# Kernel tuning notes

Hardware: AMD Instinct MI355X
Metric: run time of the kernel (lower is better)

## Reference

```python
import jax, jax.numpy as jnp
import numpy as np
from jax import lax

NAMES = ['k', 'v', 'q', 'eta', 'alpha', 'memory']
RES = {'k': True, 'v': True, 'q': True, 'eta': False, 'alpha': False, 'memory': True}
CHUNK = 16


def _mlp(x, st, residual):
    # x: (B,C,d_in); st W1:(B,d_out,d_hid) W2:(B,d_hid,d_in) b1:(B,d_out) b2:(B,d_hid)
    h = jax.nn.silu(jnp.einsum('bcd,bhd->bch', x, st['W2']) + st['b2'][:, None, :])
    out = jnp.einsum('bch,boh->bco', h, st['W1']) + st['b1'][:, None, :]
    return x + out if residual else out


def _dgd_grads(x, target, st, residual):
    # manual chain rule for L = (1/2C)||M(x)-target||^2
    C = x.shape[1]
    pre = jnp.einsum('bcd,bhd->bch', x, st['W2']) + st['b2'][:, None, :]
    sig = jax.nn.sigmoid(pre)
    h = pre * sig  # silu
    pred = jnp.einsum('bch,boh->bco', h, st['W1']) + st['b1'][:, None, :]
    if residual:
        pred = x + pred
    error = (pred - target) / C  # (B,C,d_out)
    dW1 = jnp.einsum('bco,bch->boh', error, h)
    db1 = error.sum(axis=1)
    dl_dh = jnp.einsum('bco,boh->bch', error, st['W1'])
    silu_grad = sig * (1.0 + pre * (1.0 - sig))
    dl_dpre = dl_dh * silu_grad
    dW2 = jnp.einsum('bch,bcd->bhd', dl_dpre, x)
    db2 = dl_dpre.sum(axis=1)
    return {'W1': dW1, 'W2': dW2, 'b1': db1, 'b2': db2}


def _clamp(w):
    B = w.shape[0]
    flat = w.reshape(B, -1)
    norm = jnp.linalg.norm(flat, axis=1)
    max_n = np.sqrt(flat.shape[1]).astype(np.float32)
    scale = jnp.minimum(max_n / (norm + 1e-8), 1.0)
    return w * scale.reshape((B,) + (1,) * (w.ndim - 1))


def _l2norm(x):
    return x / jnp.maximum(jnp.linalg.norm(x, axis=-1, keepdims=True), 1e-12)


def _titans(x, mods, in_W, in_b, out_W, out_b, ln_g, ln_b):
    B, T, _ = x.shape
    C = CHUNK
    NC = T // C
    z = x @ in_W.T + in_b  # (B,T,d_memory)
    zc = z.reshape(B, NC, C, -1).transpose(1, 0, 2, 3)  # (NC,B,C,d)

    states = {}
    for name in NAMES:
        W1, b1, W2, b2 = mods[name]
        states[name] = {
            'W1': jnp.broadcast_to(W1, (B,) + W1.shape),
            'b1': jnp.broadcast_to(b1, (B,) + b1.shape),
            'W2': jnp.broadcast_to(W2, (B,) + W2.shape),
            'b2': jnp.broadcast_to(b2, (B,) + b2.shape),
        }

    def step(st, z_chunk):
        k = _mlp(z_chunk, st['k'], True)
        v = _mlp(z_chunk, st['v'], True)
        q = _mlp(z_chunk, st['q'], True)
        eta = jax.nn.sigmoid(_mlp(z_chunk, st['eta'], False))    # (B,C,1)
        alpha = jax.nn.sigmoid(_mlp(z_chunk, st['alpha'], False))
        k = _l2norm(k)
        q = _l2norm(q)
        o = _mlp(q, st['memory'], True)
        ea = eta.mean(axis=1)    # (B,1)
        aa = alpha.mean(axis=1)  # (B,1)
        new = {}
        for name in NAMES:
            s = st[name]
            res = RES[name]
            v_hat = lax.stop_gradient(_mlp(v, s, res))
            g = _dgd_grads(k, v_hat, s, res)
            ns = {}
            for pn in ('W1', 'W2', 'b1', 'b2'):
                gr = g[pn]
                a = aa.reshape((aa.shape[0],) + (1,) * (gr.ndim - 1))
                e = ea.reshape((ea.shape[0],) + (1,) * (gr.ndim - 1))
                ns[pn] = _clamp(a * s[pn] - e * gr)
            new[name] = ns
        new = jax.tree.map(lax.stop_gradient, new)  # bptt_depth=0 detach
        return new, o

    _, outs = lax.scan(step, states, zc)  # outs: (NC,B,C,d)
    out = outs.transpose(1, 0, 2, 3).reshape(B, T, -1)
    mu = out.mean(axis=-1, keepdims=True)
    var = out.var(axis=-1, keepdims=True)
    out = (out - mu) / jnp.sqrt(var + 1e-5) * ln_g + ln_b
    return out @ out_W.T + out_b


def setup_inputs() -> dict:
    key = jax.random.key(0)
    B, T, Dm = 4, 2048, 1024
    Dmem = 1024
    ks = jax.random.split(key, 10)
    inp = {'x': jax.random.normal(ks[0], (B, T, Dm), jnp.float32)}
    d_outs = {'k': Dmem, 'v': Dmem, 'q': Dmem, 'eta': 1, 'alpha': 1, 'memory': Dmem}
    b1_special = {'eta': -3.0, 'alpha': 3.0}
    for i, (m, do) in enumerate(d_outs.items()):
        inp[f'{m}_W1'] = jnp.zeros((do, Dmem), jnp.float32)
        inp[f'{m}_b1'] = jnp.full((do,), b1_special.get(m, 0.0), jnp.float32)
        inp[f'{m}_W2'] = (jax.random.normal(ks[1 + i], (Dmem, Dm), jnp.float32)
                          * np.sqrt(2.0 / Dm).astype(np.float32))
        inp[f'{m}_b2'] = jnp.zeros((Dmem,), jnp.float32)
    inp['in_W'] = jax.random.normal(ks[7], (Dmem, Dm), jnp.float32) * 0.02
    inp['in_b'] = jnp.zeros((Dmem,), jnp.float32)
    inp['out_W'] = jax.random.normal(ks[8], (Dm, Dmem), jnp.float32) * 0.02
    inp['out_b'] = jnp.zeros((Dm,), jnp.float32)
    inp['ln_g'] = jnp.ones((Dmem,), jnp.float32)
    inp['ln_b'] = jnp.zeros((Dmem,), jnp.float32)
    return inp


def reference(x, k_W1, k_b1, k_W2, k_b2, v_W1, v_b1, v_W2, v_b2,
              q_W1, q_b1, q_W2, q_b2, eta_W1, eta_b1, eta_W2, eta_b2,
              alpha_W1, alpha_b1, alpha_W2, alpha_b2,
              memory_W1, memory_b1, memory_W2, memory_b2,
              in_W, in_b, out_W, out_b, ln_g, ln_b):
    mods = {
        'k': (k_W1, k_b1, k_W2, k_b2),
        'v': (v_W1, v_b1, v_W2, v_b2),
        'q': (q_W1, q_b1, q_W2, q_b2),
        'eta': (eta_W1, eta_b1, eta_W2, eta_b2),
        'alpha': (alpha_W1, alpha_b1, alpha_W2, alpha_b2),
        'memory': (memory_W1, memory_b1, memory_W2, memory_b2),
    }
    return _titans(x, mods, in_W, in_b, out_W, out_b, ln_g, ln_b)
```

## Files before the change

kernel.cpp:

```cpp
#include <hip/hip_runtime.h>
#include <math.h>

#define DI __device__ __forceinline__

namespace {

typedef unsigned short u16;
typedef unsigned int u32;
typedef __attribute__((ext_vector_type(8))) short bf8;
typedef __attribute__((ext_vector_type(4))) float f4;

DI f4 MFB(bf8 a, bf8 b, f4 c) { return __builtin_amdgcn_mfma_f32_16x16x32_bf16(a, b, c, 0, 0, 0); }

constexpr int DOUTS[6] = {1024, 1024, 1024, 1, 1, 1024};
constexpr int BIGM[4] = {0, 1, 2, 5};

constexpr long SZ_BIGM = 2100224, SZ_SMALLM = 1051648;
constexpr long MODOFF[6] = {0, SZ_BIGM, 2 * SZ_BIGM, 3 * SZ_BIGM,
                            3 * SZ_BIGM + SZ_SMALLM, 3 * SZ_BIGM + 2 * SZ_SMALLM};
constexpr long BSTRIDE = 3 * SZ_BIGM + 2 * SZ_SMALLM + SZ_BIGM;

constexpr long OFF_Z     = 0;
constexpr long OFF_STATE = 8388608;
constexpr long OFF_SPRE5 = OFF_STATE + 4 * BSTRIDE;
constexpr long OFF_KVQ   = OFF_SPRE5 + 327680;
constexpr long OFF_SPREV = OFF_KVQ + 196608;
constexpr long OFF_PREK  = OFF_SPREV + 393216;
constexpr long OFF_SPREK = OFF_PREK + 393216;
constexpr long OFF_SPREO = OFF_SPREK + 393216;
constexpr long OFF_ERR   = OFF_SPREO + 65536;
constexpr long OFF_DLP   = OFF_ERR + 393216;
constexpr long OFF_RSSQ  = OFF_DLP + 393216;
constexpr long OFF_EA    = OFF_RSSQ + 128;
constexpr long OFF_SCALE = OFF_EA + 8;
constexpr long OFF_SUMSQ = OFF_SCALE + 96;
constexpr long OFF_FLAG  = OFF_SUMSQ + 96;
constexpr long WS_FLOATS = OFF_FLAG + 8;

struct InPtrs { const float* p[31]; };

DI float* modBase(float* ws, int b, int m) {
  return ws + OFF_STATE + (long)b * BSTRIDE + MODOFF[m];
}
DI float* vecp(float* base, int m) { return base + ((m == 3 || m == 4) ? 1048576 : 2097152); }
DI int sidx(int b, int m, int p) { return ((b * 6 + m) << 2) + p; }
DI float maxnf(int m, int p) {
  switch (p) {
    case 0: return sqrtf((float)(1024 * DOUTS[m]));
    case 1: return sqrtf((float)DOUTS[m]);
    case 2: return 1024.0f;
    default: return 32.0f;
  }
}
DI float sigm(float x) { return 1.0f / (1.0f + expf(-x)); }
DI float silu(float x) { return x * sigm(x); }
DI u16 f2bf(float x) {
  u32 u = __float_as_uint(x);
  return (u16)((u + 0x7fffu + ((u >> 16) & 1u)) >> 16);
}

DI void sumsqReduce(float ss, float* slack, float* dst) {
#pragma unroll
  for (int st = 32; st >= 1; st >>= 1) ss += __shfl_xor(ss, st);
  const int tid = threadIdx.x;
  if ((tid & 63) == 0) slack[tid >> 6] = ss;
  __syncthreads();
  if (tid == 0) atomicAdd(dst, slack[0] + slack[1] + slack[2] + slack[3]);
  __syncthreads();
}

DI void split3v(const float v[8], bf8& p0, bf8& p1, bf8& p2) {
#pragma unroll
  for (int i = 0; i < 8; i++) {
    const u32 u = __float_as_uint(v[i]);
    const float f0 = __uint_as_float(u & 0xffff0000u);
    const float r1 = v[i] - f0;
    const u32 u1 = __float_as_uint(r1);
    const float f1 = __uint_as_float(u1 & 0xffff0000u);
    const float r2 = r1 - f1;
    p0[i] = (short)(u >> 16);
    p1[i] = (short)(u1 >> 16);
    p2[i] = (short)f2bf(r2);
  }
}
DI void split3p(const float* p, bf8& p0, bf8& p1, bf8& p2) {
  const float4 a = *(const float4*)p, b = *(const float4*)(p + 4);
  const float v[8] = {a.x, a.y, a.z, a.w, b.x, b.y, b.z, b.w};
  split3v(v, p0, p1, p2);
}

__global__ void k_probe(float* ws) {
  const int l = threadIdx.x, cl = l & 15, kq = l >> 4;
  bf8 af, bf_;
#pragma unroll
  for (int i = 0; i < 8; i++) { af[i] = 0; bf_[i] = 0; }
  if (kq == 0) {
    af[0] = (short)f2bf((float)(cl + 1));
    bf_[0] = (short)f2bf((float)(128 * (cl + 1)));
  }
  f4 d = MFB(af, bf_, f4{0.f, 0.f, 0.f, 0.f});
  bool m0 = true, m1 = true;
#pragma unroll
  for (int r = 0; r < 4; r++) {
    m0 = m0 && (d[r] == (float)((kq * 4 + r + 1) * 128 * (cl + 1)));
    m1 = m1 && (d[r] == (float)((cl + 1) * 128 * (kq * 4 + r + 1)));
  }
  const unsigned long long b0 = __ballot(m0), b1 = __ballot(m1);
  if (l == 0) ws[OFF_FLAG] = (b0 == ~0ull) ? 0.f : ((b1 == ~0ull) ? 1.f : 0.f);
}

template <class EF>
DI void mcK1(float* sm, const float* __restrict__ X, const float* __restrict__ W,
             int n0, int flg, EF&& ef) {
  const int tid = threadIdx.x, g = tid >> 6, l = tid & 63, cl = l & 15, kq = l >> 4;
  f4 acc = {0.f, 0.f, 0.f, 0.f};
  const float* Xr = X + (long)cl * 1024 + g * 256 + kq * 8;
  const float* Wr = W + (long)(n0 + cl) * 1024 + g * 256 + kq * 8;
#pragma unroll 2
  for (int ch = 0; ch < 8; ch++) {
    bf8 x0, x1, x2, w0, w1, w2;
    split3p(Xr + ch * 32, x0, x1, x2);
    split3p(Wr + ch * 32, w0, w1, w2);
    acc = MFB(x2, w0, acc); acc = MFB(x1, w1, acc); acc = MFB(x0, w2, acc);
    acc = MFB(x1, w0, acc); acc = MFB(x0, w1, acc); acc = MFB(x0, w0, acc);
  }
  *(f4*)(sm + g * 256 + l * 4) = acc;
  __syncthreads();
  const int le = tid >> 2, re = tid & 3;
  const float v = sm[le * 4 + re] + sm[256 + le * 4 + re] +
                  sm[512 + le * 4 + re] + sm[768 + le * 4 + re];
  const int ccl = le & 15, ckq = le >> 4;
  const int c = flg ? ccl : ckq * 4 + re;
  const int n = n0 + (flg ? ckq * 4 + re : ccl);
  ef(c, n, v);
}

template <class EF>
DI void mcK2(float* sm, const float* __restrict__ X1, const float* __restrict__ X2,
             const float* __restrict__ W, int n0, int flg, EF&& ef) {
  const int tid = threadIdx.x, g = tid >> 6, l = tid & 63, cl = l & 15, kq = l >> 4;
  f4 a1 = {0.f, 0.f, 0.f, 0.f}, a2 = {0.f, 0.f, 0.f, 0.f};
  const float* X1r = X1 + (long)cl * 1024 + g * 256 + kq * 8;
  const float* X2r = X2 + (long)cl * 1024 + g * 256 + kq * 8;
  const float* Wr = W + (long)(n0 + cl) * 1024 + g * 256 + kq * 8;
#pragma unroll 2
  for (int ch = 0; ch < 8; ch++) {
    bf8 w0, w1, w2, x0, x1, x2, y0, y1, y2;
    split3p(Wr + ch * 32, w0, w1, w2);
    split3p(X1r + ch * 32, x0, x1, x2);
    split3p(X2r + ch * 32, y0, y1, y2);
    a1 = MFB(x2, w0, a1); a1 = MFB(x1, w1, a1); a1 = MFB(x0, w2, a1);
    a1 = MFB(x1, w0, a1); a1 = MFB(x0, w1, a1); a1 = MFB(x0, w0, a1);
    a2 = MFB(y2, w0, a2); a2 = MFB(y1, w1, a2); a2 = MFB(y0, w2, a2);
    a2 = MFB(y1, w0, a2); a2 = MFB(y0, w1, a2); a2 = MFB(y0, w0, a2);
  }
  *(f4*)(sm + g * 256 + l * 4) = a1;
  *(f4*)(sm + 1024 + g * 256 + l * 4) = a2;
  __syncthreads();
  const int le = tid >> 2, re = tid & 3;
  const float v1 = sm[le * 4 + re] + sm[256 + le * 4 + re] +
                   sm[512 + le * 4 + re] + sm[768 + le * 4 + re];
  const float v2 = sm[1024 + le * 4 + re] + sm[1280 + le * 4 + re] +
                   sm[1536 + le * 4 + re] + sm[1792 + le * 4 + re];
  const int ccl = le & 15, ckq = le >> 4;
  const int c = flg ? ccl : ckq * 4 + re;
  const int n = n0 + (flg ? ckq * 4 + re : ccl);
  ef(c, n, v1, v2);
}

template <class EF>
DI void mcK1t(float* sm, const float* __restrict__ E, const float* __restrict__ W1,
              int h0, int flg, EF&& ef) {
  const int tid = threadIdx.x, g = tid >> 6, l = tid & 63, cl = l & 15, kq = l >> 4;
  f4 acc = {0.f, 0.f, 0.f, 0.f};
  const float* Er = E + (long)cl * 1024 + g * 256 + kq * 8;
  const float* Wc = W1 + (long)(g * 256 + kq * 8) * 1024 + h0 + cl;
#pragma unroll 2
  for (int ch = 0; ch < 8; ch++) {
    bf8 x0, x1, x2, w0, w1, w2;
    split3p(Er + ch * 32, x0, x1, x2);
    float v[8];
#pragma unroll
    for (int i = 0; i < 8; i++) v[i] = Wc[(long)(ch * 32 + i) * 1024];
    split3v(v, w0, w1, w2);
    acc = MFB(x2, w0, acc); acc = MFB(x1, w1, acc); acc = MFB(x0, w2, acc);
    acc = MFB(x1, w0, acc); acc = MFB(x0, w1, acc); acc = MFB(x0, w0, acc);
  }
  *(f4*)(sm + g * 256 + l * 4) = acc;
  __syncthreads();
  const int le = tid >> 2, re = tid & 3;
  const float v = sm[le * 4 + re] + sm[256 + le * 4 + re] +
                  sm[512 + le * 4 + re] + sm[768 + le * 4 + re];
  const int ccl = le & 15, ckq = le >> 4;
  const int c = flg ? ccl : ckq * 4 + re;
  const int h = h0 + (flg ? ckq * 4 + re : ccl);
  ef(c, h, v);
}


__global__ __launch_bounds__(256) void k_p0(float* ws, InPtrs in) {
  const long i = threadIdx.x + (long)blockIdx.x * 256;
  if (i < 96) { ws[OFF_SCALE + i] = 1.f; return; }
  if (i < 192) { ws[OFF_SUMSQ + (i - 96)] = 0.f; return; }
  if (i < 320) { ws[OFF_RSSQ + (i - 192)] = 0.f; return; }
  const long j = i - 320;
  if (j < 24 * 2048) {
    const int bm = (int)(j >> 11), q = (int)(j & 2047);
    const int b = bm / 6, m = bm % 6;
    float* vc = vecp(modBase(ws, b, m), m);
    if (q < 1024) { if (q < DOUTS[m]) vc[q] = in.p[2 + 4 * m][q]; }
    else vc[1024 + (q - 1024)] = in.p[4 + 4 * m][q - 1024];
    return;
  }
  const long j2 = j - 49152;
  if (j2 < 8192) {
    const int e = (int)(j2 >> 10), b = e >> 1, m = 3 + (e & 1);
    const int h = (int)(j2 & 1023);
    vecp(modBase(ws, b, m), m)[2048 + h] = in.p[1 + 4 * m][h];
  }
}

__global__ __launch_bounds__(256) void k_pc(float* ws, InPtrs in) {
  const int bid = blockIdx.x, job = bid >> 9, sub = bid & 511;
  const long e0 = (long)sub * 2048 + threadIdx.x * 8;
  int m; bool w1;
  if (job < 6) { m = job; w1 = false; }
  else { m = BIGM[job - 6]; w1 = true; }
  const float* src = in.p[(w1 ? 1 : 3) + 4 * m];
  const float4 a = *(const float4*)(src + e0);
  const float4 b4 = *(const float4*)(src + e0 + 4);
#pragma unroll
  for (int q = 0; q < 4; q++) {
    float* dst = modBase(ws, q, m) + (w1 ? 1048576 : 0);
    *(float4*)(dst + e0) = a;
    *(float4*)(dst + e0 + 4) = b4;
  }
}

__global__ __launch_bounds__(256) void k_gbig(const float* __restrict__ X,
                                              const float* __restrict__ A,
                                              const float* __restrict__ bias,
                                              float* __restrict__ Y,
                                              const float* flagp) {
  __shared__ float sm[1024];
  const int bid = blockIdx.x, nb = bid & 63;
  const long rb = bid >> 6;
  const int flg = (int)flagp[0];
  const float* Xr = X + rb * 16 * 1024;
  float* Yr = Y + rb * 16 * 1024;
  mcK1(sm, Xr, A, nb * 16, flg, [&](int c, int n, float v) {
    Yr[(long)c * 1024 + n] = v + bias[n];
  });
}


__global__ __launch_bounds__(256) void k_s0(float* ws) {
  const int i = threadIdx.x;
  if (i < 96) {
    const float ssv = ws[OFF_SUMSQ + i];
    const int p = i & 3, m = (i >> 2) % 6;
    ws[OFF_SCALE + i] = fminf(maxnf(m, p) / (sqrtf(ssv) + 1e-8f), 1.0f);
    ws[OFF_SUMSQ + i] = 0.f;
  } else if (i < 224) {
    ws[OFF_RSSQ + (i - 96)] = 0.f;
  }
}

__global__ __launch_bounds__(256) void k_s1(float* ws, int t) {
  __shared__ float sm[1024];
  const int bid = blockIdx.x, n0 = (bid & 63) * 16, m = (bid >> 6) % 5, b = bid / 320;
  const int flg = (int)ws[OFF_FLAG];
  const float* zc = ws + OFF_Z + ((long)b * 2048 + (long)t * 16) * 1024;
  float* base = modBase(ws, b, m);
  const float cW2 = ws[OFF_SCALE + sidx(b, m, 2)], cb2 = ws[OFF_SCALE + sidx(b, m, 3)];
  const float* b2v = vecp(base, m) + 1024;
  float* Y = ws + OFF_SPRE5 + ((long)b * 5 + m) * 16384;
  mcK1(sm, zc, base, n0, flg, [&](int c, int n, float v) {
    Y[(long)c * 1024 + n] = silu(fmaf(cW2, v, cb2 * b2v[n]));
  });
}

__global__ __launch_bounds__(256) void k_s2(float* ws, int t) {
  __shared__ float sm[1024 + 16 + 64];
  float* smr = sm + 1024;
  float* sm2 = sm + 1040;
  const int tid = threadIdx.x, bid = blockIdx.x;
  if (bid < 768) {
    const int n0 = (bid & 63) * 16, m = (bid >> 6) % 3, b = bid / 192;
    const int flg = (int)ws[OFF_FLAG];
    if (tid < 16) smr[tid] = 0.f;
    const float* spre = ws + OFF_SPRE5 + ((long)b * 5 + m) * 16384;
    float* base = modBase(ws, b, m);
    const float* zc = ws + OFF_Z + ((long)b * 2048 + (long)t * 16) * 1024;
    const float cW1 = ws[OFF_SCALE + sidx(b, m, 0)], cb1 = ws[OFF_SCALE + sidx(b, m, 1)];
    const float* b1v = vecp(base, m);
    float* out = ws + OFF_KVQ + ((long)b * 3 + m) * 16384;
    const bool sq = (m != 1);
    mcK1(sm, spre, base + 1048576, n0, flg, [&](int c, int n, float v) {
      const float val = fmaf(cW1, v, fmaf(cb1, b1v[n], zc[(long)c * 1024 + n]));
      out[(long)c * 1024 + n] = val;
      if (sq) atomicAdd(&smr[c], val * val);
    });
    __syncthreads();
    if (sq && tid < 16)
      atomicAdd(ws + OFF_RSSQ + (long)b * 32 + (m == 0 ? 0 : 16) + tid, smr[tid]);
  } else {
    const int e = bid - 768, b = e >> 1, m = 3 + (e & 1);
    const float* spre = ws + OFF_SPRE5 + ((long)b * 5 + m) * 16384;
    float* base = modBase(ws, b, m);
    const float* w1 = vecp(base, m) + 2048;
    float av[16];
#pragma unroll
    for (int c = 0; c < 16; c++) av[c] = 0.f;
    for (int jj = 0; jj < 4; jj++) {
      const int h = tid + 256 * jj;
      const float w = w1[h];
#pragma unroll
      for (int c = 0; c < 16; c++) av[c] = fmaf(spre[c * 1024 + h], w, av[c]);
    }
#pragma unroll
    for (int st = 1; st < 64; st <<= 1)
#pragma unroll
      for (int c = 0; c < 16; c++) av[c] += __shfl_xor(av[c], st);
    if ((tid & 63) == 0) {
      const int w4 = tid >> 6;
#pragma unroll
      for (int c = 0; c < 16; c++) sm2[w4 * 16 + c] = av[c];
    }
    __syncthreads();
    if (tid == 0) {
      const float cW1 = ws[OFF_SCALE + sidx(b, m, 0)], cb1 = ws[OFF_SCALE + sidx(b, m, 1)];
      const float b10 = vecp(base, m)[0];
      float s = 0.f;
      for (int c = 0; c < 16; c++) {
        const float tot = sm2[c] + sm2[16 + c] + sm2[32 + c] + sm2[48 + c];
        s += sigm(fmaf(cW1, tot, cb1 * b10));
      }
      ws[OFF_EA + ((m == 3) ? 0 : 4) + b] = s * 0.0625f;
    }
  }
}

__global__ __launch_bounds__(256) void k_s3(float* ws) {
  __shared__ float sm[2048 + 16];
  float* sminv = sm + 2048;
  const int bid = blockIdx.x, tid = threadIdx.x;
  const int flg = (int)ws[OFF_FLAG];
  if (bid < 1536) {
    const int n0 = (bid & 63) * 16, m = (bid >> 6) % 6, b = bid / 384;
    if (tid < 16)
      sminv[tid] = 1.f / fmaxf(sqrtf(ws[OFF_RSSQ + (long)b * 32 + tid]), 1e-12f);
    const float* vX = ws + OFF_KVQ + ((long)b * 3 + 1) * 16384;
    const float* kX = ws + OFF_KVQ + ((long)b * 3 + 0) * 16384;
    float* base = modBase(ws, b, m);
    const float cW2 = ws[OFF_SCALE + sidx(b, m, 2)], cb2 = ws[OFF_SCALE + sidx(b, m, 3)];
    const float* b2v = vecp(base, m) + 1024;
    float* Ysv = ws + OFF_SPREV + ((long)b * 6 + m) * 16384;
    float* Yk = ws + OFF_PREK + ((long)b * 6 + m) * 16384;
    float* Ysk = ws + OFF_SPREK + ((long)b * 6 + m) * 16384;
    mcK2(sm, vX, kX, base, n0, flg, [&](int c, int n, float v1, float v2) {
      const float bb = cb2 * b2v[n];
      Ysv[(long)c * 1024 + n] = silu(fmaf(cW2, v1, bb));
      const float pk = fmaf(cW2 * sminv[c], v2, bb);
      Yk[(long)c * 1024 + n] = pk;
      Ysk[(long)c * 1024 + n] = silu(pk);
    });
  } else {
    const int id = bid - 1536, n0 = (id & 63) * 16, b = id >> 6;
    if (tid < 16)
      sminv[tid] = 1.f / fmaxf(sqrtf(ws[OFF_RSSQ + (long)b * 32 + 16 + tid]), 1e-12f);
    const float* qX = ws + OFF_KVQ + ((long)b * 3 + 2) * 16384;
    float* base = modBase(ws, b, 5);
    const float cW2 = ws[OFF_SCALE + sidx(b, 5, 2)], cb2 = ws[OFF_SCALE + sidx(b, 5, 3)];
    const float* b2v = vecp(base, 5) + 1024;
    float* Y = ws + OFF_SPREO + (long)b * 16384;
    mcK1(sm, qX, base, n0, flg, [&](int c, int n, float v) {
      Y[(long)c * 1024 + n] = silu(fmaf(cW2 * sminv[c], v, cb2 * b2v[n]));
    });
  }
}

__global__ __launch_bounds__(256) void k_s4(float* ws, int t) {
  __shared__ float sm[2048 + 16 + 128];
  float* sminv = sm + 2048;
  float* sm4 = sm + 2064;
  const int tid = threadIdx.x, bid = blockIdx.x;
  if (bid < 1024) {
    const int n0 = (bid & 63) * 16, mi = (bid >> 6) & 3, b = bid >> 8;
    const int m = BIGM[mi];
    const int flg = (int)ws[OFF_FLAG];
    if (tid < 16)
      sminv[tid] = 1.f / fmaxf(sqrtf(ws[OFF_RSSQ + (long)b * 32 + tid]), 1e-12f);
    const float* sprev = ws + OFF_SPREV + ((long)b * 6 + m) * 16384;
    const float* sprek = ws + OFF_SPREK + ((long)b * 6 + m) * 16384;
    float* base = modBase(ws, b, m);
    const float cW1 = ws[OFF_SCALE + sidx(b, m, 0)], cb1 = ws[OFF_SCALE + sidx(b, m, 1)];
    const float* b1v = vecp(base, m);
    const float* vraw = ws + OFF_KVQ + ((long)b * 3 + 1) * 16384;
    const float* kraw = ws + OFF_KVQ + ((long)b * 3 + 0) * 16384;
    float* errP = ws + OFF_ERR + ((long)b * 6 + m) * 16384;
    mcK2(sm, sprev, sprek, base + 1048576, n0, flg, [&](int c, int n, float v1, float v2) {
      const float bbb = cb1 * b1v[n];
      const float vh = fmaf(cW1, v1, bbb + vraw[(long)c * 1024 + n]);
      const float pr = fmaf(cW1, v2, bbb + kraw[(long)c * 1024 + n] * sminv[c]);
      errP[(long)c * 1024 + n] = (pr - vh) * 0.0625f;
    });
  } else if (bid < 1280) {
    const int id = bid - 1024, n0 = (id & 63) * 16, b = id >> 6;
    const int flg = (int)ws[OFF_FLAG];
    if (tid < 16)
      sminv[tid] = 1.f / fmaxf(sqrtf(ws[OFF_RSSQ + (long)b * 32 + 16 + tid]), 1e-12f);
    const float* spreo = ws + OFF_SPREO + (long)b * 16384;
    float* base = modBase(ws, b, 5);
    const float cW1 = ws[OFF_SCALE + sidx(b, 5, 0)], cb1 = ws[OFF_SCALE + sidx(b, 5, 1)];
    const float* b1v = vecp(base, 5);
    const float* qraw = ws + OFF_KVQ + ((long)b * 3 + 2) * 16384;
    float* zc = ws + OFF_Z + ((long)b * 2048 + (long)t * 16) * 1024;
    mcK1(sm, spreo, base + 1048576, n0, flg, [&](int c, int n, float v) {
      zc[(long)c * 1024 + n] = fmaf(cW1, v, cb1 * b1v[n] + qraw[(long)c * 1024 + n] * sminv[c]);
    });
  } else {
    const int id = bid - 1280, b = id >> 1, m = 3 + (id & 1);
    const float* sprev = ws + OFF_SPREV + ((long)b * 6 + m) * 16384;
    const float* sprek = ws + OFF_SPREK + ((long)b * 6 + m) * 16384;
    float* base = modBase(ws, b, m);
    const float* w1 = vecp(base, m) + 2048;
    float av[16], ap[16];
#pragma unroll
    for (int c = 0; c < 16; c++) { av[c] = 0.f; ap[c] = 0.f; }
    for (int jj = 0; jj < 4; jj++) {
      const int h = tid + 256 * jj;
      const float w = w1[h];
#pragma unroll
      for (int c = 0; c < 16; c++) {
        av[c] = fmaf(sprev[c * 1024 + h], w, av[c]);
        ap[c] = fmaf(sprek[c * 1024 + h], w, ap[c]);
      }
    }
#pragma unroll
    for (int st = 1; st < 64; st <<= 1)
#pragma unroll
      for (int c = 0; c < 16; c++) {
        av[c] += __shfl_xor(av[c], st);
        ap[c] += __shfl_xor(ap[c], st);
      }
    if ((tid & 63) == 0) {
      const int w4 = tid >> 6;
#pragma unroll
      for (int c = 0; c < 16; c++) { sm4[w4 * 32 + c] = av[c]; sm4[w4 * 32 + 16 + c] = ap[c]; }
    }
    __syncthreads();
    if (tid == 0) {
      const float cW1 = ws[OFF_SCALE + sidx(b, m, 0)], cb1 = ws[OFF_SCALE + sidx(b, m, 1)];
      const float b10 = vecp(base, m)[0];
      float* errP = ws + OFF_ERR + ((long)b * 6 + m) * 16384;
      for (int c = 0; c < 16; c++) {
        const float sv = sm4[c] + sm4[32 + c] + sm4[64 + c] + sm4[96 + c];
        const float sp = sm4[16 + c] + sm4[48 + c] + sm4[80 + c] + sm4[112 + c];
        errP[c * 1024] = (fmaf(cW1, sp, cb1 * b10) - fmaf(cW1, sv, cb1 * b10)) * 0.0625f;
      }
    }
  }
}

__global__ __launch_bounds__(256) void k_s5(float* ws) {
  __shared__ float sm[1024];
  const int tid = threadIdx.x, bid = blockIdx.x;
  if (bid < 1024) {
    const int h0 = (bid & 63) * 16, mi = (bid >> 6) & 3, b = bid >> 8;
    const int m = BIGM[mi];
    const int flg = (int)ws[OFF_FLAG];
    float* base = modBase(ws, b, m);
    const float* errP = ws + OFF_ERR + ((long)b * 6 + m) * 16384;
    const float cW1 = ws[OFF_SCALE + sidx(b, m, 0)];
    const float* prek = ws + OFF_PREK + ((long)b * 6 + m) * 16384;
    float* dlp = ws + OFF_DLP + ((long)b * 6 + m) * 16384;
    mcK1t(sm, errP, base + 1048576, h0, flg, [&](int c, int h, float v) {
      const float pre = prek[(long)c * 1024 + h];
      const float sg = sigm(pre);
      dlp[(long)c * 1024 + h] = cW1 * v * (sg * (1.f + pre * (1.f - sg)));
    });
  } else {
    const int e = bid - 1024, sub = e & 3, bm = e >> 2, b = bm >> 1, m = 3 + (bm & 1);
    const float cW1 = ws[OFF_SCALE + sidx(b, m, 0)];
    const float* errP = ws + OFF_ERR + ((long)b * 6 + m) * 16384;
    const float* prek = ws + OFF_PREK + ((long)b * 6 + m) * 16384;
    const float* w1 = vecp(modBase(ws, b, m), m) + 2048;
    float* dlp = ws + OFF_DLP + ((long)b * 6 + m) * 16384;
    for (int i = tid; i < 4096; i += 256) {
      const long idx = (long)sub * 4096 + i;
      const int c = (int)(idx >> 10), h = (int)(idx & 1023);
      const float pre = prek[idx];
      const float sg = sigm(pre);
      dlp[idx] = errP[c * 1024] * cW1 * w1[h] * (sg * (1.f + pre * (1.f - sg)));
    }
  }
}

__global__ __launch_bounds__(256) void k_s6(float* ws) {
  __shared__ float sm[64 * 20 + 8];
  float* slack = sm + 64 * 20;
  const int tid = threadIdx.x, bid = blockIdx.x;
  if (bid < 640) {
    const bool isW2 = bid < 384;
    int b, m, r0, scaleIdx;
    float* W;
    float4 fac[16];
    const float* tsrc;
    if (isW2) {
      const int bm = bid >> 4;
      b = bm / 6; m = bm % 6; r0 = (bid & 15) * 64;
      W = modBase(ws, b, m);
      scaleIdx = sidx(b, m, 2);
      tsrc = ws + OFF_DLP + ((long)b * 6 + m) * 16384;
      const float* kraw = ws + OFF_KVQ + ((long)b * 3) * 16384;
#pragma unroll
      for (int c = 0; c < 16; c++) {
        const float inv = 1.f / fmaxf(sqrtf(ws[OFF_RSSQ + (long)b * 32 + c]), 1e-12f);
        const float4 kk = *(const float4*)(kraw + (long)c * 1024 + tid * 4);
        fac[c].x = kk.x * inv; fac[c].y = kk.y * inv;
        fac[c].z = kk.z * inv; fac[c].w = kk.w * inv;
      }
    } else {
      const int id = bid - 384, bm = id >> 4;
      b = bm >> 2; m = BIGM[bm & 3]; r0 = (id & 15) * 64;
      W = modBase(ws, b, m) + 1048576;
      scaleIdx = sidx(b, m, 0);
      tsrc = ws + OFF_ERR + ((long)b * 6 + m) * 16384;
      const float* sprek = ws + OFF_SPREK + ((long)b * 6 + m) * 16384;
#pragma unroll
      for (int c = 0; c < 16; c++)
        fac[c] = *(const float4*)(sprek + (long)c * 1024 + tid * 4);
    }
    for (int f = tid; f < 1024; f += 256) {
      const int c = f >> 6, hh = f & 63;
      sm[hh * 20 + c] = tsrc[(long)c * 1024 + r0 + hh];
    }
    __syncthreads();
    const float ea = ws[OFF_EA + b], aa = ws[OFF_EA + 4 + b];
    const float ac = aa * ws[OFF_SCALE + scaleIdx];
    float ss = 0.f;
#pragma unroll 1
    for (int hh = 0; hh < 64; hh++) {
      const float4 q0 = *(const float4*)(sm + hh * 20);
      const float4 q1 = *(const float4*)(sm + hh * 20 + 4);
      const float4 q2 = *(const float4*)(sm + hh * 20 + 8);
      const float4 q3 = *(const float4*)(sm + hh * 20 + 12);
      float4 g = {0.f, 0.f, 0.f, 0.f};
#pragma unroll
      for (int c = 0; c < 16; c++) {
        const float4 qq = c < 4 ? q0 : (c < 8 ? q1 : (c < 12 ? q2 : q3));
        const float dv = (&qq.x)[c & 3];
        g.x = fmaf(dv, fac[c].x, g.x);
        g.y = fmaf(dv, fac[c].y, g.y);
        g.z = fmaf(dv, fac[c].z, g.z);
        g.w = fmaf(dv, fac[c].w, g.w);
      }
      float4* Wp = (float4*)(W + (size_t)(r0 + hh) * 1024 + tid * 4);
      float4 w = *Wp;
      w.x = fmaf(ac, w.x, -ea * g.x);
      w.y = fmaf(ac, w.y, -ea * g.y);
      w.z = fmaf(ac, w.z, -ea * g.z);
      w.w = fmaf(ac, w.w, -ea * g.w);
      *Wp = w;
      ss = fmaf(w.x, w.x, fmaf(w.y, w.y, fmaf(w.z, w.z, fmaf(w.w, w.w, ss))));
    }
    sumsqReduce(ss, slack, ws + OFF_SUMSQ + scaleIdx);
  } else if (bid < 688) {
    const int id = bid - 640;
    const int b = id / 12, r = id % 12, m = r >> 1, which = r & 1;
    const float ea = ws[OFF_EA + b], aa = ws[OFF_EA + 4 + b];
    float* vc = vecp(modBase(ws, b, m), m);
    float ss = 0.f;
    if (which == 0) {
      const int n = DOUTS[m];
      const float* errP = ws + OFF_ERR + ((long)b * 6 + m) * 16384;
      const float ac = aa * ws[OFF_SCALE + sidx(b, m, 1)];
      for (int o = tid; o < n; o += 256) {
        float gs = 0.f;
#pragma unroll
        for (int c = 0; c < 16; c++) gs += errP[c * 1024 + o];
        const float nw = fmaf(ac, vc[o], -ea * gs);
        vc[o] = nw;
        ss = fmaf(nw, nw, ss);
      }
      sumsqReduce(ss, slack, ws + OFF_SUMSQ + sidx(b, m, 1));
    } else {
      const float* dlpP = ws + OFF_DLP + ((long)b * 6 + m) * 16384;
      const float ac = aa * ws[OFF_SCALE + sidx(b, m, 3)];
      for (int h = tid; h < 1024; h += 256) {
        float gs = 0.f;
#pragma unroll
        for (int c = 0; c < 16; c++) gs += dlpP[c * 1024 + h];
        const float nw = fmaf(ac, vc[1024 + h], -ea * gs);
        vc[1024 + h] = nw;
        ss = fmaf(nw, nw, ss);
      }
      sumsqReduce(ss, slack, ws + OFF_SUMSQ + sidx(b, m, 3));
    }
  } else {
    const int e2 = bid - 688, b = e2 >> 1, m = 3 + (e2 & 1);
    const float ea = ws[OFF_EA + b], aa = ws[OFF_EA + 4 + b];
    float* vc = vecp(modBase(ws, b, m), m);
    const float* errP = ws + OFF_ERR + ((long)b * 6 + m) * 16384;
    const float* sprek = ws + OFF_SPREK + ((long)b * 6 + m) * 16384;
    const float ac = aa * ws[OFF_SCALE + sidx(b, m, 0)];
    float ss = 0.f;
    for (int h = tid; h < 1024; h += 256) {
      float gs = 0.f;
#pragma unroll
      for (int c = 0; c < 16; c++)
        gs = fmaf(errP[c * 1024], sprek[c * 1024 + h], gs);
      const float nw = fmaf(ac, vc[2048 + h], -ea * gs);
      vc[2048 + h] = nw;
      ss = fmaf(nw, nw, ss);
    }
    sumsqReduce(ss, slack, ws + OFF_SUMSQ + sidx(b, m, 0));
  }
}


__global__ __launch_bounds__(256) void k_ln(float* ws, const float* __restrict__ g,
                                            const float* __restrict__ bb) {
  __shared__ float sm[8];
  float* p = ws + OFF_Z + (long)blockIdx.x * 1024;
  const int tid = threadIdx.x;
  float s = 0.f, s2 = 0.f;
  for (int j = tid; j < 1024; j += 256) {
    const float v = p[j];
    s += v;
    s2 = fmaf(v, v, s2);
  }
#pragma unroll
  for (int st = 32; st >= 1; st >>= 1) { s += __shfl_xor(s, st); s2 += __shfl_xor(s2, st); }
  if ((tid & 63) == 0) { sm[tid >> 6] = s; sm[4 + (tid >> 6)] = s2; }
  __syncthreads();
  const float S = sm[0] + sm[1] + sm[2] + sm[3];
  const float S2 = sm[4] + sm[5] + sm[6] + sm[7];
  const float mu = S * (1.f / 1024.f);
  const float var = S2 * (1.f / 1024.f) - mu * mu;
  const float inv = 1.f / sqrtf(var + 1e-5f);
  for (int j = tid; j < 1024; j += 256) {
    p[j] = fmaf((p[j] - mu) * inv, g[j], bb[j]);
  }
}

}

extern "C" void kernel_launch(void* const* d_in, const int* in_sizes, int n_in,
                              void* d_out, int out_size, void* d_ws, size_t ws_size,
                              hipStream_t stream) {
  (void)in_sizes; (void)n_in; (void)out_size;
  if (ws_size < (size_t)WS_FLOATS * sizeof(float)) return;
  float* ws = (float*)d_ws;
  InPtrs ip;
  for (int i = 0; i < 31; i++) ip.p[i] = (const float*)d_in[i];

  k_probe<<<1, 64, 0, stream>>>(ws);
  k_p0<<<256, 256, 0, stream>>>(ws, ip);
  k_pc<<<5120, 256, 0, stream>>>(ws, ip);
  k_gbig<<<32768, 256, 0, stream>>>((const float*)d_in[0], (const float*)d_in[25],
                                    (const float*)d_in[26], ws + OFF_Z, ws + OFF_FLAG);

  for (int t = 0; t < 128; t++) {
    if (t) k_s0<<<1, 256, 0, stream>>>(ws);
    k_s1<<<1280, 256, 0, stream>>>(ws, t);
    k_s2<<<776, 256, 0, stream>>>(ws, t);
    k_s3<<<1792, 256, 0, stream>>>(ws);
    k_s4<<<1288, 256, 0, stream>>>(ws, t);
    k_s5<<<1056, 256, 0, stream>>>(ws);
    k_s6<<<696, 256, 0, stream>>>(ws);
  }

  k_ln<<<8192, 256, 0, stream>>>(ws, (const float*)d_in[29], (const float*)d_in[30]);
  k_gbig<<<32768, 256, 0, stream>>>(ws + OFF_Z, (const float*)d_in[27],
                                    (const float*)d_in[28], (float*)d_out, ws + OFF_FLAG);
}
```

Baseline: 25.37 ms.

## Defer weight updates into next step's matmul kernels with analytic norm tracking

```diff
diff --git a/kernel.cpp b/kernel.cpp
--- a/kernel.cpp
+++ b/kernel.cpp
@@ -20,22 +20,25 @@
                             3 * SZ_BIGM + SZ_SMALLM, 3 * SZ_BIGM + 2 * SZ_SMALLM};
 constexpr long BSTRIDE = 3 * SZ_BIGM + 2 * SZ_SMALLM + SZ_BIGM;
 
-constexpr long OFF_Z     = 0;
-constexpr long OFF_STATE = 8388608;
-constexpr long OFF_SPRE5 = OFF_STATE + 4 * BSTRIDE;
-constexpr long OFF_KVQ   = OFF_SPRE5 + 327680;
-constexpr long OFF_SPREV = OFF_KVQ + 196608;
-constexpr long OFF_PREK  = OFF_SPREV + 393216;
-constexpr long OFF_SPREK = OFF_PREK + 393216;
-constexpr long OFF_SPREO = OFF_SPREK + 393216;
-constexpr long OFF_ERR   = OFF_SPREO + 65536;
-constexpr long OFF_DLP   = OFF_ERR + 393216;
-constexpr long OFF_RSSQ  = OFF_DLP + 393216;
-constexpr long OFF_EA    = OFF_RSSQ + 128;
-constexpr long OFF_SCALE = OFF_EA + 8;
-constexpr long OFF_SUMSQ = OFF_SCALE + 96;
-constexpr long OFF_FLAG  = OFF_SUMSQ + 96;
-constexpr long WS_FLOATS = OFF_FLAG + 8;
+constexpr long OFF_Z       = 0;
+constexpr long OFF_STATE   = 8388608;
+constexpr long OFF_SPRE5   = OFF_STATE + 4 * BSTRIDE;
+constexpr long OFF_KVQ     = OFF_SPRE5 + 327680;
+constexpr long OFF_SPREV   = OFF_KVQ + 196608;
+constexpr long OFF_PREK    = OFF_SPREV + 393216;
+constexpr long OFF_SPREK   = OFF_PREK + 393216;
+constexpr long OFF_SPREO   = OFF_SPREK + 393216;
+constexpr long OFF_ERR     = OFF_SPREO + 65536;
+constexpr long OFF_DLP     = OFF_ERR + 393216;
+constexpr long OFF_PREKRAW = OFF_DLP + 393216;
+constexpr long OFF_RAWPK   = OFF_PREKRAW + 393216;
+constexpr long OFF_RSSQ    = OFF_RAWPK + 262144;
+constexpr long OFF_EA      = OFF_RSSQ + 256;
+constexpr long OFF_SCALE   = OFF_EA + 16;
+constexpr long OFF_SUMSQ   = OFF_SCALE + 192;
+constexpr long OFF_NORMSQ  = OFF_SUMSQ + 96;
+constexpr long OFF_FLAG    = OFF_NORMSQ + 96;
+constexpr long WS_FLOATS   = OFF_FLAG + 8;
 
 struct InPtrs { const float* p[31]; };
 
@@ -110,7 +113,7 @@
 }
 
 template <class EF>
-DI void mcK1(float* sm, const float* __restrict__ X, const float* __restrict__ W,
+DI void mcK1(float* sm, const float* __restrict__ X, const float* W,
              int n0, int flg, EF&& ef) {
   const int tid = threadIdx.x, g = tid >> 6, l = tid & 63, cl = l & 15, kq = l >> 4;
   f4 acc = {0.f, 0.f, 0.f, 0.f};
@@ -137,7 +140,7 @@
 
 template <class EF>
 DI void mcK2(float* sm, const float* __restrict__ X1, const float* __restrict__ X2,
-             const float* __restrict__ W, int n0, int flg, EF&& ef) {
+             const float* W, int n0, int flg, EF&& ef) {
   const int tid = threadIdx.x, g = tid >> 6, l = tid & 63, cl = l & 15, kq = l >> 4;
   f4 a1 = {0.f, 0.f, 0.f, 0.f}, a2 = {0.f, 0.f, 0.f, 0.f};
   const float* X1r = X1 + (long)cl * 1024 + g * 256 + kq * 8;
@@ -169,7 +172,7 @@
 }
 
 template <class EF>
-DI void mcK1t(float* sm, const float* __restrict__ E, const float* __restrict__ W1,
+DI void mcK1t(float* sm, const float* __restrict__ E, const float* W1,
               int h0, int flg, EF&& ef) {
   const int tid = threadIdx.x, g = tid >> 6, l = tid & 63, cl = l & 15, kq = l >> 4;
   f4 acc = {0.f, 0.f, 0.f, 0.f};
@@ -197,13 +200,39 @@
   ef(c, h, v);
 }
 
+DI void updTile(float* W, int n0, const float* coefS, const float4* fac,
+                float ac, float ea) {
+  const int tid = threadIdx.x;
+#pragma unroll 1
+  for (int hh = 0; hh < 16; hh++) {
+    float4 g = {0.f, 0.f, 0.f, 0.f};
+#pragma unroll
+    for (int c = 0; c < 16; c++) {
+      const float dv = coefS[c * 16 + hh];
+      g.x = fmaf(dv, fac[c].x, g.x);
+      g.y = fmaf(dv, fac[c].y, g.y);
+      g.z = fmaf(dv, fac[c].z, g.z);
+      g.w = fmaf(dv, fac[c].w, g.w);
+    }
+    float4* Wp = (float4*)(W + (size_t)(n0 + hh) * 1024 + tid * 4);
+    float4 w = *Wp;
+    w.x = fmaf(ac, w.x, -ea * g.x);
+    w.y = fmaf(ac, w.y, -ea * g.y);
+    w.z = fmaf(ac, w.z, -ea * g.z);
+    w.w = fmaf(ac, w.w, -ea * g.w);
+    *Wp = w;
+  }
+}
+
 
 __global__ __launch_bounds__(256) void k_p0(float* ws, InPtrs in) {
   const long i = threadIdx.x + (long)blockIdx.x * 256;
-  if (i < 96) { ws[OFF_SCALE + i] = 1.f; return; }
-  if (i < 192) { ws[OFF_SUMSQ + (i - 96)] = 0.f; return; }
-  if (i < 320) { ws[OFF_RSSQ + (i - 192)] = 0.f; return; }
-  const long j = i - 320;
+  if (i < 192) { ws[OFF_SCALE + i] = 1.f; return; }
+  if (i < 288) { ws[OFF_SUMSQ + (i - 192)] = 0.f; return; }
+  if (i < 384) { ws[OFF_NORMSQ + (i - 288)] = 0.f; return; }
+  if (i < 640) { ws[OFF_RSSQ + (i - 384)] = 0.f; return; }
+  if (i < 656) { ws[OFF_EA + (i - 640)] = 0.f; return; }
+  const long j = i - 656;
   if (j < 24 * 2048) {
     const int bm = (int)(j >> 11), q = (int)(j & 2047);
     const int b = bm / 6, m = bm % 6;
@@ -237,8 +266,30 @@
   }
 }
 
+__global__ __launch_bounds__(256) void k_pn(float* ws, InPtrs in) {
+  __shared__ float slack[8];
+  const int bid = blockIdx.x, job = bid >> 6, r0 = (bid & 63) * 16, tid = threadIdx.x;
+  const int m = (job < 5) ? job : job - 5;
+  const bool w1 = job >= 5;
+  const float* src = in.p[(w1 ? 1 : 3) + 4 * m];
+  float ss = 0.f;
+#pragma unroll 1
+  for (int r = 0; r < 16; r++) {
+    const float4 v = *(const float4*)(src + (size_t)(r0 + r) * 1024 + tid * 4);
+    ss = fmaf(v.x, v.x, fmaf(v.y, v.y, fmaf(v.z, v.z, fmaf(v.w, v.w, ss))));
+  }
+  sumsqReduce(ss, slack, ws + OFF_NORMSQ + sidx(0, m, w1 ? 0 : 2));
+}
+__global__ void k_pn2(float* ws) {
+  const int tid = threadIdx.x;
+  if (tid >= 24) return;
+  const int s = tid / 3, b = tid % 3 + 1;
+  const int m = (s < 5) ? s : s - 5, p = (s < 5) ? 2 : 0;
+  ws[OFF_NORMSQ + sidx(b, m, p)] = ws[OFF_NORMSQ + sidx(0, m, p)];
+}
+
 __global__ __launch_bounds__(256) void k_gbig(const float* __restrict__ X,
-                                              const float* __restrict__ A,
+                                              const float* A,
                                               const float* __restrict__ bias,
                                               float* __restrict__ Y,
                                               const float* flagp) {
@@ -254,56 +305,224 @@
 }
 
 
-__global__ __launch_bounds__(256) void k_s0(float* ws) {
-  const int i = threadIdx.x;
-  if (i < 96) {
-    const float ssv = ws[OFF_SUMSQ + i];
-    const int p = i & 3, m = (i >> 2) % 6;
-    ws[OFF_SCALE + i] = fminf(maxnf(m, p) / (sqrtf(ssv) + 1e-8f), 1.0f);
-    ws[OFF_SUMSQ + i] = 0.f;
-  } else if (i < 224) {
-    ws[OFF_RSSQ + (i - 96)] = 0.f;
+__global__ __launch_bounds__(256) void k_K0(float* ws, int t) {
+  __shared__ float sm[160];
+  const int tid = threadIdx.x, bid = blockIdx.x;
+  const int pc = t & 1, pp = (t - 1) & 1;
+  const float* eaP = ws + OFF_EA + pp * 8;
+  const float* sclP = ws + OFF_SCALE + pp * 96;
+  float* sclC = ws + OFF_SCALE + pc * 96;
+  if (bid < 32) {
+    int b, m, slot;
+    const float *A, *R;
+    const float *B;
+    bool isW2;
+    if (bid < 20) {
+      b = bid / 5; m = bid % 5; slot = sidx(b, m, 2); isW2 = true;
+      A = ws + OFF_DLP + ((long)b * 6 + m) * 16384;
+      R = ws + OFF_PREKRAW + ((long)b * 6 + m) * 16384;
+      B = ws + OFF_KVQ + (long)b * 3 * 16384;
+    } else {
+      const int id = bid - 20;
+      b = id / 3; m = id % 3; slot = sidx(b, m, 0); isW2 = false;
+      A = ws + OFF_ERR + ((long)b * 6 + m) * 16384;
+      R = ws + OFF_RAWPK + ((long)b * 4 + m) * 16384;
+      B = ws + OFF_SPREK + ((long)b * 6 + m) * 16384;
+    }
+    float dp = 0.f;
+    for (int i = tid; i < 16384; i += 256) dp = fmaf(A[i], R[i], dp);
+#pragma unroll
+    for (int st = 32; st >= 1; st >>= 1) dp += __shfl_xor(dp, st);
+    if ((tid & 63) == 0) sm[tid >> 6] = dp;
+    __syncthreads();
+    if (tid < 136) {
+      int c = 0, p = tid;
+      while (p >= 16 - c) { p -= 16 - c; c++; }
+      const int c2 = c + p;
+      float invc = 1.f, invc2 = 1.f;
+      if (isW2) {
+        const float* rs = ws + OFF_RSSQ + pp * 128 + (long)b * 32;
+        invc = 1.f / fmaxf(sqrtf(rs[c]), 1e-12f);
+        invc2 = 1.f / fmaxf(sqrtf(rs[c2]), 1e-12f);
+      }
+      float ga = 0.f, gb = 0.f;
+      const float *Ac = A + (long)c * 1024, *Ac2 = A + (long)c2 * 1024;
+      const float *Bc = B + (long)c * 1024, *Bc2 = B + (long)c2 * 1024;
+      for (int d = 0; d < 1024; d++) {
+        ga = fmaf(Ac[d], Ac2[d], ga);
+        gb = fmaf(Bc[d], Bc2[d], gb);
+      }
+      gb *= invc * invc2;
+      sm[8 + tid] = (c == c2 ? 1.f : 2.f) * ga * gb;
+    }
+    __syncthreads();
+    if (tid == 0) {
+      double dot = (double)sm[0] + sm[1] + sm[2] + sm[3];
+      double gg = 0.0;
+      for (int i = 0; i < 136; i++) gg += (double)sm[8 + i];
+      const double ea = (double)eaP[b], aa = (double)eaP[4 + b];
+      const double ac = aa * (double)sclP[slot];
+      double S = ac * ac * (double)ws[OFF_NORMSQ + slot] - 2.0 * ac * ea * dot +
+                 ea * ea * gg;
+      if (S < 0.0) S = 0.0;
+      ws[OFF_NORMSQ + slot] = (float)S;
+      sclC[slot] = fminf(maxnf(m, isW2 ? 2 : 0) / ((float)sqrt(S) + 1e-8f), 1.0f);
+    }
+  } else if (bid < 40) {
+    if (tid == 0) {
+      const int e = bid - 32, b = e >> 1, p = (e & 1) ? 0 : 2;
+      const int slot = sidx(b, 5, p);
+      const float S = ws[OFF_SUMSQ + slot];
+      sclC[slot] = fminf(maxnf(5, p) / (sqrtf(S) + 1e-8f), 1.0f);
+      ws[OFF_SUMSQ + slot] = 0.f;
+    }
+  } else if (bid < 96) {
+    const int id = bid - 40;
+    int b, m, kind;
+    if (id < 24) { b = id / 6; m = id % 6; kind = 0; }
+    else if (id < 48) { const int q = id - 24; b = q / 6; m = q % 6; kind = 1; }
+    else { const int q = id - 48; b = q >> 1; m = 3 + (q & 1); kind = 2; }
+    const float ea = eaP[b], aa = eaP[4 + b];
+    float* vc = vecp(modBase(ws, b, m), m);
+    if (kind == 0 && DOUTS[m] == 1) {
+      if (tid == 0) {
+        const float* errP = ws + OFF_ERR + ((long)b * 6 + m) * 16384;
+        float g = 0.f;
+        for (int c = 0; c < 16; c++) g += errP[c * 1024];
+        const float nv = fmaf(aa, vc[0], -ea * g);
+        const float sc = fminf(1.0f / (fabsf(nv) + 1e-8f), 1.0f);
+        vc[0] = sc * nv;
+      }
+      return;
+    }
+    float nv[4];
+    float ss = 0.f;
+    const int o = tid * 4;
+    if (kind == 0) {
+      const float* errP = ws + OFF_ERR + ((long)b * 6 + m) * 16384;
+#pragma unroll
+      for (int j = 0; j < 4; j++) {
+        float g = 0.f;
+        for (int c = 0; c < 16; c++) g += errP[c * 1024 + o + j];
+        nv[j] = fmaf(aa, vc[o + j], -ea * g);
+        ss = fmaf(nv[j], nv[j], ss);
+      }
+    } else if (kind == 1) {
+      const float* dlpP = ws + OFF_DLP + ((long)b * 6 + m) * 16384;
+#pragma unroll
+      for (int j = 0; j < 4; j++) {
+        float g = 0.f;
+        for (int c = 0; c < 16; c++) g += dlpP[c * 1024 + o + j];
+        nv[j] = fmaf(aa, vc[1024 + o + j], -ea * g);
+        ss = fmaf(nv[j], nv[j], ss);
+      }
+    } else {
+      const float* errP = ws + OFF_ERR + ((long)b * 6 + m) * 16384;
+      const float* sprek = ws + OFF_SPREK + ((long)b * 6 + m) * 16384;
+      float e0[16];
+#pragma unroll
+      for (int c = 0; c < 16; c++) e0[c] = errP[c * 1024];
+#pragma unroll
+      for (int j = 0; j < 4; j++) {
+        float g = 0.f;
+        for (int c = 0; c < 16; c++) g = fmaf(e0[c], sprek[c * 1024 + o + j], g);
+        nv[j] = fmaf(aa, vc[2048 + o + j], -ea * g);
+        ss = fmaf(nv[j], nv[j], ss);
+      }
+    }
+#pragma unroll
+    for (int st = 32; st >= 1; st >>= 1) ss += __shfl_xor(ss, st);
+    if ((tid & 63) == 0) sm[tid >> 6] = ss;
+    __syncthreads();
+    const float S = sm[0] + sm[1] + sm[2] + sm[3];
+    const float mx = (kind == 0) ? maxnf(m, 1) : 32.0f;
+    const float sc = fminf(mx / (sqrtf(S) + 1e-8f), 1.0f);
+    const long off = (kind == 0) ? 0 : (kind == 1 ? 1024 : 2048);
+#pragma unroll
+    for (int j = 0; j < 4; j++) vc[off + o + j] = sc * nv[j];
+  } else {
+    if (tid < 128) ws[OFF_RSSQ + pc * 128 + tid] = 0.f;
   }
 }
 
 __global__ __launch_bounds__(256) void k_s1(float* ws, int t) {
-  __shared__ float sm[1024];
-  const int bid = blockIdx.x, n0 = (bid & 63) * 16, m = (bid >> 6) % 5, b = bid / 320;
+  __shared__ float sm[1024 + 256];
+  const int bid = blockIdx.x, tid = threadIdx.x;
+  const int n0 = (bid & 63) * 16, m = (bid >> 6) % 5, b = bid / 320;
   const int flg = (int)ws[OFF_FLAG];
+  const int pc = t & 1, pp = (t - 1) & 1;
+  float* base = modBase(ws, b, m);
+  if (t > 0) {
+    const float* eaP = ws + OFF_EA + pp * 8;
+    const float ac = eaP[4 + b] * ws[OFF_SCALE + pp * 96 + sidx(b, m, 2)];
+    const float ea = eaP[b];
+    const float* kraw = ws + OFF_KVQ + (long)b * 3 * 16384;
+    const float* rs = ws + OFF_RSSQ + pp * 128 + (long)b * 32;
+    float4 fac[16];
+#pragma unroll
+    for (int c = 0; c < 16; c++) {
+      const float inv = 1.f / fmaxf(sqrtf(rs[c]), 1e-12f);
+      const float4 kk = *(const float4*)(kraw + (long)c * 1024 + tid * 4);
+      fac[c].x = kk.x * inv; fac[c].y = kk.y * inv;
+      fac[c].z = kk.z * inv; fac[c].w = kk.w * inv;
+    }
+    const float* dlpP = ws + OFF_DLP + ((long)b * 6 + m) * 16384;
+    sm[1024 + tid] = dlpP[(long)(tid >> 4) * 1024 + n0 + (tid & 15)];
+    __syncthreads();
+    updTile(base, n0, sm + 1024, fac, ac, ea);
+    __syncthreads();
+  }
   const float* zc = ws + OFF_Z + ((long)b * 2048 + (long)t * 16) * 1024;
-  float* base = modBase(ws, b, m);
-  const float cW2 = ws[OFF_SCALE + sidx(b, m, 2)], cb2 = ws[OFF_SCALE + sidx(b, m, 3)];
+  const float cW2 = ws[OFF_SCALE + pc * 96 + sidx(b, m, 2)];
   const float* b2v = vecp(base, m) + 1024;
   float* Y = ws + OFF_SPRE5 + ((long)b * 5 + m) * 16384;
   mcK1(sm, zc, base, n0, flg, [&](int c, int n, float v) {
-    Y[(long)c * 1024 + n] = silu(fmaf(cW2, v, cb2 * b2v[n]));
+    Y[(long)c * 1024 + n] = silu(fmaf(cW2, v, b2v[n]));
   });
 }
 
 __global__ __launch_bounds__(256) void k_s2(float* ws, int t) {
-  __shared__ float sm[1024 + 16 + 64];
-  float* smr = sm + 1024;
-  float* sm2 = sm + 1040;
+  __shared__ float sm[1024 + 256 + 16 + 64];
+  float* coefS = sm + 1024;
+  float* smr = sm + 1280;
+  float* sm2 = sm + 1296;
   const int tid = threadIdx.x, bid = blockIdx.x;
+  const int pc = t & 1, pp = (t - 1) & 1;
   if (bid < 768) {
     const int n0 = (bid & 63) * 16, m = (bid >> 6) % 3, b = bid / 192;
     const int flg = (int)ws[OFF_FLAG];
+    float* base = modBase(ws, b, m);
+    if (t > 0) {
+      const float* eaP = ws + OFF_EA + pp * 8;
+      const float ac = eaP[4 + b] * ws[OFF_SCALE + pp * 96 + sidx(b, m, 0)];
+      const float ea = eaP[b];
+      const float* sprek = ws + OFF_SPREK + ((long)b * 6 + m) * 16384;
+      float4 fac[16];
+#pragma unroll
+      for (int c = 0; c < 16; c++)
+        fac[c] = *(const float4*)(sprek + (long)c * 1024 + tid * 4);
+      const float* errP = ws + OFF_ERR + ((long)b * 6 + m) * 16384;
+      coefS[tid] = errP[(long)(tid >> 4) * 1024 + n0 + (tid & 15)];
+      __syncthreads();
+      updTile(base + 1048576, n0, coefS, fac, ac, ea);
+      __syncthreads();
+    }
     if (tid < 16) smr[tid] = 0.f;
     const float* spre = ws + OFF_SPRE5 + ((long)b * 5 + m) * 16384;
-    float* base = modBase(ws, b, m);
     const float* zc = ws + OFF_Z + ((long)b * 2048 + (long)t * 16) * 1024;
-    const float cW1 = ws[OFF_SCALE + sidx(b, m, 0)], cb1 = ws[OFF_SCALE + sidx(b, m, 1)];
+    const float cW1 = ws[OFF_SCALE + pc * 96 + sidx(b, m, 0)];
     const float* b1v = vecp(base, m);
     float* out = ws + OFF_KVQ + ((long)b * 3 + m) * 16384;
     const bool sq = (m != 1);
     mcK1(sm, spre, base + 1048576, n0, flg, [&](int c, int n, float v) {
-      const float val = fmaf(cW1, v, fmaf(cb1, b1v[n], zc[(long)c * 1024 + n]));
+      const float val = fmaf(cW1, v, b1v[n] + zc[(long)c * 1024 + n]);
       out[(long)c * 1024 + n] = val;
       if (sq) atomicAdd(&smr[c], val * val);
     });
     __syncthreads();
     if (sq && tid < 16)
-      atomicAdd(ws + OFF_RSSQ + (long)b * 32 + (m == 0 ? 0 : 16) + tid, smr[tid]);
+      atomicAdd(ws + OFF_RSSQ + pc * 128 + (long)b * 32 + (m == 0 ? 0 : 16) + tid,
+                smr[tid]);
   } else {
     const int e = bid - 768, b = e >> 1, m = 3 + (e & 1);
     const float* spre = ws + OFF_SPRE5 + ((long)b * 5 + m) * 16384;
@@ -329,53 +548,56 @@
     }
     __syncthreads();
     if (tid == 0) {
-      const float cW1 = ws[OFF_SCALE + sidx(b, m, 0)], cb1 = ws[OFF_SCALE + sidx(b, m, 1)];
       const float b10 = vecp(base, m)[0];
       float s = 0.f;
       for (int c = 0; c < 16; c++) {
         const float tot = sm2[c] + sm2[16 + c] + sm2[32 + c] + sm2[48 + c];
-        s += sigm(fmaf(cW1, tot, cb1 * b10));
-      }
-      ws[OFF_EA + ((m == 3) ? 0 : 4) + b] = s * 0.0625f;
-    }
-  }
-}
-
-__global__ __launch_bounds__(256) void k_s3(float* ws) {
+        s += sigm(tot + b10);
+      }
+      ws[OFF_EA + pc * 8 + ((m == 3) ? 0 : 4) + b] = s * 0.0625f;
+    }
+  }
+}
+
+__global__ __launch_bounds__(256) void k_s3(float* ws, int t) {
   __shared__ float sm[2048 + 16];
   float* sminv = sm + 2048;
   const int bid = blockIdx.x, tid = threadIdx.x;
   const int flg = (int)ws[OFF_FLAG];
+  const int pc = t & 1;
   if (bid < 1536) {
     const int n0 = (bid & 63) * 16, m = (bid >> 6) % 6, b = bid / 384;
     if (tid < 16)
-      sminv[tid] = 1.f / fmaxf(sqrtf(ws[OFF_RSSQ + (long)b * 32 + tid]), 1e-12f);
+      sminv[tid] = 1.f / fmaxf(sqrtf(ws[OFF_RSSQ + pc * 128 + (long)b * 32 + tid]), 1e-12f);
     const float* vX = ws + OFF_KVQ + ((long)b * 3 + 1) * 16384;
     const float* kX = ws + OFF_KVQ + ((long)b * 3 + 0) * 16384;
     float* base = modBase(ws, b, m);
-    const float cW2 = ws[OFF_SCALE + sidx(b, m, 2)], cb2 = ws[OFF_SCALE + sidx(b, m, 3)];
+    const float cW2 = ws[OFF_SCALE + pc * 96 + sidx(b, m, 2)];
     const float* b2v = vecp(base, m) + 1024;
     float* Ysv = ws + OFF_SPREV + ((long)b * 6 + m) * 16384;
     float* Yk = ws + OFF_PREK + ((long)b * 6 + m) * 16384;
     float* Ysk = ws + OFF_SPREK + ((long)b * 6 + m) * 16384;
+    float* Ykr = ws + OFF_PREKRAW + ((long)b * 6 + m) * 16384;
     mcK2(sm, vX, kX, base, n0, flg, [&](int c, int n, float v1, float v2) {
-      const float bb = cb2 * b2v[n];
+      const float bb = b2v[n];
       Ysv[(long)c * 1024 + n] = silu(fmaf(cW2, v1, bb));
-      const float pk = fmaf(cW2 * sminv[c], v2, bb);
+      const float raw = v2 * sminv[c];
+      Ykr[(long)c * 1024 + n] = raw;
+      const float pk = fmaf(cW2, raw, bb);
       Yk[(long)c * 1024 + n] = pk;
       Ysk[(long)c * 1024 + n] = silu(pk);
     });
   } else {
     const int id = bid - 1536, n0 = (id & 63) * 16, b = id >> 6;
     if (tid < 16)
-      sminv[tid] = 1.f / fmaxf(sqrtf(ws[OFF_RSSQ + (long)b * 32 + 16 + tid]), 1e-12f);
+      sminv[tid] = 1.f / fmaxf(sqrtf(ws[OFF_RSSQ + pc * 128 + (long)b * 32 + 16 + tid]), 1e-12f);
     const float* qX = ws + OFF_KVQ + ((long)b * 3 + 2) * 16384;
     float* base = modBase(ws, b, 5);
-    const float cW2 = ws[OFF_SCALE + sidx(b, 5, 2)], cb2 = ws[OFF_SCALE + sidx(b, 5, 3)];
+    const float cW2 = ws[OFF_SCALE + pc * 96 + sidx(b, 5, 2)];
     const float* b2v = vecp(base, 5) + 1024;
     float* Y = ws + OFF_SPREO + (long)b * 16384;
     mcK1(sm, qX, base, n0, flg, [&](int c, int n, float v) {
-      Y[(long)c * 1024 + n] = silu(fmaf(cW2 * sminv[c], v, cb2 * b2v[n]));
+      Y[(long)c * 1024 + n] = silu(fmaf(cW2 * sminv[c], v, b2v[n]));
     });
   }
 }
@@ -385,39 +607,42 @@
   float* sminv = sm + 2048;
   float* sm4 = sm + 2064;
   const int tid = threadIdx.x, bid = blockIdx.x;
+  const int pc = t & 1;
   if (bid < 1024) {
     const int n0 = (bid & 63) * 16, mi = (bid >> 6) & 3, b = bid >> 8;
     const int m = BIGM[mi];
     const int flg = (int)ws[OFF_FLAG];
     if (tid < 16)
-      sminv[tid] = 1.f / fmaxf(sqrtf(ws[OFF_RSSQ + (long)b * 32 + tid]), 1e-12f);
+      sminv[tid] = 1.f / fmaxf(sqrtf(ws[OFF_RSSQ + pc * 128 + (long)b * 32 + tid]), 1e-12f);
     const float* sprev = ws + OFF_SPREV + ((long)b * 6 + m) * 16384;
     const float* sprek = ws + OFF_SPREK + ((long)b * 6 + m) * 16384;
     float* base = modBase(ws, b, m);
-    const float cW1 = ws[OFF_SCALE + sidx(b, m, 0)], cb1 = ws[OFF_SCALE + sidx(b, m, 1)];
+    const float cW1 = ws[OFF_SCALE + pc * 96 + sidx(b, m, 0)];
     const float* b1v = vecp(base, m);
     const float* vraw = ws + OFF_KVQ + ((long)b * 3 + 1) * 16384;
     const float* kraw = ws + OFF_KVQ + ((long)b * 3 + 0) * 16384;
     float* errP = ws + OFF_ERR + ((long)b * 6 + m) * 16384;
+    float* rawP = ws + OFF_RAWPK + ((long)b * 4 + mi) * 16384;
     mcK2(sm, sprev, sprek, base + 1048576, n0, flg, [&](int c, int n, float v1, float v2) {
-      const float bbb = cb1 * b1v[n];
+      const float bbb = b1v[n];
       const float vh = fmaf(cW1, v1, bbb + vraw[(long)c * 1024 + n]);
       const float pr = fmaf(cW1, v2, bbb + kraw[(long)c * 1024 + n] * sminv[c]);
+      rawP[(long)c * 1024 + n] = v2;
       errP[(long)c * 1024 + n] = (pr - vh) * 0.0625f;
     });
   } else if (bid < 1280) {
     const int id = bid - 1024, n0 = (id & 63) * 16, b = id >> 6;
     const int flg = (int)ws[OFF_FLAG];
     if (tid < 16)
-      sminv[tid] = 1.f / fmaxf(sqrtf(ws[OFF_RSSQ + (long)b * 32 + 16 + tid]), 1e-12f);
+      sminv[tid] = 1.f / fmaxf(sqrtf(ws[OFF_RSSQ + pc * 128 + (long)b * 32 + 16 + tid]), 1e-12f);
     const float* spreo = ws + OFF_SPREO + (long)b * 16384;
     float* base = modBase(ws, b, 5);
-    const float cW1 = ws[OFF_SCALE + sidx(b, 5, 0)], cb1 = ws[OFF_SCALE + sidx(b, 5, 1)];
+    const float cW1 = ws[OFF_SCALE + pc * 96 + sidx(b, 5, 0)];
     const float* b1v = vecp(base, 5);
     const float* qraw = ws + OFF_KVQ + ((long)b * 3 + 2) * 16384;
     float* zc = ws + OFF_Z + ((long)b * 2048 + (long)t * 16) * 1024;
     mcK1(sm, spreo, base + 1048576, n0, flg, [&](int c, int n, float v) {
-      zc[(long)c * 1024 + n] = fmaf(cW1, v, cb1 * b1v[n] + qraw[(long)c * 1024 + n] * sminv[c]);
+      zc[(long)c * 1024 + n] = fmaf(cW1, v, b1v[n] + qraw[(long)c * 1024 + n] * sminv[c]);
     });
   } else {
     const int id = bid - 1280, b = id >> 1, m = 3 + (id & 1);
@@ -451,28 +676,27 @@
     }
     __syncthreads();
     if (tid == 0) {
-      const float cW1 = ws[OFF_SCALE + sidx(b, m, 0)], cb1 = ws[OFF_SCALE + sidx(b, m, 1)];
-      const float b10 = vecp(base, m)[0];
       float* errP = ws + OFF_ERR + ((long)b * 6 + m) * 16384;
       for (int c = 0; c < 16; c++) {
         const float sv = sm4[c] + sm4[32 + c] + sm4[64 + c] + sm4[96 + c];
         const float sp = sm4[16 + c] + sm4[48 + c] + sm4[80 + c] + sm4[112 + c];
-        errP[c * 1024] = (fmaf(cW1, sp, cb1 * b10) - fmaf(cW1, sv, cb1 * b10)) * 0.0625f;
-      }
-    }
-  }
-}
-
-__global__ __launch_bounds__(256) void k_s5(float* ws) {
+        errP[c * 1024] = (sp - sv) * 0.0625f;
+      }
+    }
+  }
+}
+
+__global__ __launch_bounds__(256) void k_s5(float* ws, int t) {
   __shared__ float sm[1024];
   const int tid = threadIdx.x, bid = blockIdx.x;
+  const int pc = t & 1;
   if (bid < 1024) {
     const int h0 = (bid & 63) * 16, mi = (bid >> 6) & 3, b = bid >> 8;
     const int m = BIGM[mi];
     const int flg = (int)ws[OFF_FLAG];
     float* base = modBase(ws, b, m);
     const float* errP = ws + OFF_ERR + ((long)b * 6 + m) * 16384;
-    const float cW1 = ws[OFF_SCALE + sidx(b, m, 0)];
+    const float cW1 = ws[OFF_SCALE + pc * 96 + sidx(b, m, 0)];
     const float* prek = ws + OFF_PREK + ((long)b * 6 + m) * 16384;
     float* dlp = ws + OFF_DLP + ((long)b * 6 + m) * 16384;
     mcK1t(sm, errP, base + 1048576, h0, flg, [&](int c, int h, float v) {
@@ -482,7 +706,6 @@
     });
   } else {
     const int e = bid - 1024, sub = e & 3, bm = e >> 2, b = bm >> 1, m = 3 + (bm & 1);
-    const float cW1 = ws[OFF_SCALE + sidx(b, m, 0)];
     const float* errP = ws + OFF_ERR + ((long)b * 6 + m) * 16384;
     const float* prek = ws + OFF_PREK + ((long)b * 6 + m) * 16384;
     const float* w1 = vecp(modBase(ws, b, m), m) + 2048;
@@ -490,133 +713,75 @@
     for (int i = tid; i < 4096; i += 256) {
       const long idx = (long)sub * 4096 + i;
       const int c = (int)(idx >> 10), h = (int)(idx & 1023);
+      const float e0 = errP[c * 1024];
       const float pre = prek[idx];
       const float sg = sigm(pre);
-      dlp[idx] = errP[c * 1024] * cW1 * w1[h] * (sg * (1.f + pre * (1.f - sg)));
-    }
-  }
-}
-
-__global__ __launch_bounds__(256) void k_s6(float* ws) {
-  __shared__ float sm[64 * 20 + 8];
-  float* slack = sm + 64 * 20;
+      dlp[idx] = e0 * w1[h] * (sg * (1.f + pre * (1.f - sg)));
+    }
+  }
+}
+
+__global__ __launch_bounds__(256) void k_s6(float* ws, int t) {
+  __shared__ float sm[256 + 8];
+  float* slack = sm + 256;
   const int tid = threadIdx.x, bid = blockIdx.x;
-  if (bid < 640) {
-    const bool isW2 = bid < 384;
-    int b, m, r0, scaleIdx;
-    float* W;
-    float4 fac[16];
-    const float* tsrc;
-    if (isW2) {
-      const int bm = bid >> 4;
-      b = bm / 6; m = bm % 6; r0 = (bid & 15) * 64;
-      W = modBase(ws, b, m);
-      scaleIdx = sidx(b, m, 2);
-      tsrc = ws + OFF_DLP + ((long)b * 6 + m) * 16384;
-      const float* kraw = ws + OFF_KVQ + ((long)b * 3) * 16384;
-#pragma unroll
-      for (int c = 0; c < 16; c++) {
-        const float inv = 1.f / fmaxf(sqrtf(ws[OFF_RSSQ + (long)b * 32 + c]), 1e-12f);
-        const float4 kk = *(const float4*)(kraw + (long)c * 1024 + tid * 4);
-        fac[c].x = kk.x * inv; fac[c].y = kk.y * inv;
-        fac[c].z = kk.z * inv; fac[c].w = kk.w * inv;
-      }
-    } else {
-      const int id = bid - 384, bm = id >> 4;
-      b = bm >> 2; m = BIGM[bm & 3]; r0 = (id & 15) * 64;
-      W = modBase(ws, b, m) + 1048576;
-      scaleIdx = sidx(b, m, 0);
-      tsrc = ws + OFF_ERR + ((long)b * 6 + m) * 16384;
-      const float* sprek = ws + OFF_SPREK + ((long)b * 6 + m) * 16384;
-#pragma unroll
-      for (int c = 0; c < 16; c++)
-        fac[c] = *(const float4*)(sprek + (long)c * 1024 + tid * 4);
-    }
-    for (int f = tid; f < 1024; f += 256) {
-      const int c = f >> 6, hh = f & 63;
-      sm[hh * 20 + c] = tsrc[(long)c * 1024 + r0 + hh];
-    }
-    __syncthreads();
-    const float ea = ws[OFF_EA + b], aa = ws[OFF_EA + 4 + b];
-    const float ac = aa * ws[OFF_SCALE + scaleIdx];
-    float ss = 0.f;
+  const int pc = t & 1;
+  const bool isW2 = bid < 256;
+  const int b = (bid & 255) >> 6, n0 = (bid & 63) * 16;
+  float* base = modBase(ws, b, 5);
+  const float* eaC = ws + OFF_EA + pc * 8;
+  const float ea = eaC[b], aa = eaC[4 + b];
+  float* W;
+  float4 fac[16];
+  int slot;
+  if (isW2) {
+    W = base;
+    slot = sidx(b, 5, 2);
+    const float* kraw = ws + OFF_KVQ + (long)b * 3 * 16384;
+    const float* rs = ws + OFF_RSSQ + pc * 128 + (long)b * 32;
+#pragma unroll
+    for (int c = 0; c < 16; c++) {
+      const float inv = 1.f / fmaxf(sqrtf(rs[c]), 1e-12f);
+      const float4 kk = *(const float4*)(kraw + (long)c * 1024 + tid * 4);
+      fac[c].x = kk.x * inv; fac[c].y = kk.y * inv;
+      fac[c].z = kk.z * inv; fac[c].w = kk.w * inv;
+    }
+    const float* dlpP = ws + OFF_DLP + ((long)b * 6 + 5) * 16384;
+    sm[tid] = dlpP[(long)(tid >> 4) * 1024 + n0 + (tid & 15)];
+  } else {
+    W = base + 1048576;
+    slot = sidx(b, 5, 0);
+    const float* sprek = ws + OFF_SPREK + ((long)b * 6 + 5) * 16384;
+#pragma unroll
+    for (int c = 0; c < 16; c++)
+      fac[c] = *(const float4*)(sprek + (long)c * 1024 + tid * 4);
+    const float* errP = ws + OFF_ERR + ((long)b * 6 + 5) * 16384;
+    sm[tid] = errP[(long)(tid >> 4) * 1024 + n0 + (tid & 15)];
+  }
+  __syncthreads();
+  const float ac = aa * ws[OFF_SCALE + pc * 96 + slot];
+  float ss = 0.f;
 #pragma unroll 1
-    for (int hh = 0; hh < 64; hh++) {
-      const float4 q0 = *(const float4*)(sm + hh * 20);
-      const float4 q1 = *(const float4*)(sm + hh * 20 + 4);
-      const float4 q2 = *(const float4*)(sm + hh * 20 + 8);
-      const float4 q3 = *(const float4*)(sm + hh * 20 + 12);
-      float4 g = {0.f, 0.f, 0.f, 0.f};
-#pragma unroll
-      for (int c = 0; c < 16; c++) {
-        const float4 qq = c < 4 ? q0 : (c < 8 ? q1 : (c < 12 ? q2 : q3));
-        const float dv = (&qq.x)[c & 3];
-        g.x = fmaf(dv, fac[c].x, g.x);
-        g.y = fmaf(dv, fac[c].y, g.y);
-        g.z = fmaf(dv, fac[c].z, g.z);
-        g.w = fmaf(dv, fac[c].w, g.w);
-      }
-      float4* Wp = (float4*)(W + (size_t)(r0 + hh) * 1024 + tid * 4);
-      float4 w = *Wp;
-      w.x = fmaf(ac, w.x, -ea * g.x);
-      w.y = fmaf(ac, w.y, -ea * g.y);
-      w.z = fmaf(ac, w.z, -ea * g.z);
-      w.w = fmaf(ac, w.w, -ea * g.w);
-      *Wp = w;
-      ss = fmaf(w.x, w.x, fmaf(w.y, w.y, fmaf(w.z, w.z, fmaf(w.w, w.w, ss))));
-    }
-    sumsqReduce(ss, slack, ws + OFF_SUMSQ + scaleIdx);
-  } else if (bid < 688) {
-    const int id = bid - 640;
-    const int b = id / 12, r = id % 12, m = r >> 1, which = r & 1;
-    const float ea = ws[OFF_EA + b], aa = ws[OFF_EA + 4 + b];
-    float* vc = vecp(modBase(ws, b, m), m);
-    float ss = 0.f;
-    if (which == 0) {
-      const int n = DOUTS[m];
-      const float* errP = ws + OFF_ERR + ((long)b * 6 + m) * 16384;
-      const float ac = aa * ws[OFF_SCALE + sidx(b, m, 1)];
-      for (int o = tid; o < n; o += 256) {
-        float gs = 0.f;
-#pragma unroll
-        for (int c = 0; c < 16; c++) gs += errP[c * 1024 + o];
-        const float nw = fmaf(ac, vc[o], -ea * gs);
-        vc[o] = nw;
-        ss = fmaf(nw, nw, ss);
-      }
-      sumsqReduce(ss, slack, ws + OFF_SUMSQ + sidx(b, m, 1));
-    } else {
-      const float* dlpP = ws + OFF_DLP + ((long)b * 6 + m) * 16384;
-      const float ac = aa * ws[OFF_SCALE + sidx(b, m, 3)];
-      for (int h = tid; h < 1024; h += 256) {
-        float gs = 0.f;
-#pragma unroll
-        for (int c = 0; c < 16; c++) gs += dlpP[c * 1024 + h];
-        const float nw = fmaf(ac, vc[1024 + h], -ea * gs);
-        vc[1024 + h] = nw;
-        ss = fmaf(nw, nw, ss);
-      }
-      sumsqReduce(ss, slack, ws + OFF_SUMSQ + sidx(b, m, 3));
-    }
-  } else {
-    const int e2 = bid - 688, b = e2 >> 1, m = 3 + (e2 & 1);
-    const float ea = ws[OFF_EA + b], aa = ws[OFF_EA + 4 + b];
-    float* vc = vecp(modBase(ws, b, m), m);
-    const float* errP = ws + OFF_ERR + ((long)b * 6 + m) * 16384;
-    const float* sprek = ws + OFF_SPREK + ((long)b * 6 + m) * 16384;
-    const float ac = aa * ws[OFF_SCALE + sidx(b, m, 0)];
-    float ss = 0.f;
-    for (int h = tid; h < 1024; h += 256) {
-      float gs = 0.f;
-#pragma unroll
-      for (int c = 0; c < 16; c++)
-        gs = fmaf(errP[c * 1024], sprek[c * 1024 + h], gs);
-      const float nw = fmaf(ac, vc[2048 + h], -ea * gs);
-      vc[2048 + h] = nw;
-      ss = fmaf(nw, nw, ss);
-    }
-    sumsqReduce(ss, slack, ws + OFF_SUMSQ + sidx(b, m, 0));
-  }
+  for (int hh = 0; hh < 16; hh++) {
+    float4 g = {0.f, 0.f, 0.f, 0.f};
+#pragma unroll
+    for (int c = 0; c < 16; c++) {
+      const float dv = sm[c * 16 + hh];
+      g.x = fmaf(dv, fac[c].x, g.x);
+      g.y = fmaf(dv, fac[c].y, g.y);
+      g.z = fmaf(dv, fac[c].z, g.z);
+      g.w = fmaf(dv, fac[c].w, g.w);
+    }
+    float4* Wp = (float4*)(W + (size_t)(n0 + hh) * 1024 + tid * 4);
+    float4 w = *Wp;
+    w.x = fmaf(ac, w.x, -ea * g.x);
+    w.y = fmaf(ac, w.y, -ea * g.y);
+    w.z = fmaf(ac, w.z, -ea * g.z);
+    w.w = fmaf(ac, w.w, -ea * g.w);
+    *Wp = w;
+    ss = fmaf(w.x, w.x, fmaf(w.y, w.y, fmaf(w.z, w.z, fmaf(w.w, w.w, ss))));
+  }
+  sumsqReduce(ss, slack, ws + OFF_SUMSQ + slot);
 }
 
 
@@ -659,17 +824,19 @@
   k_probe<<<1, 64, 0, stream>>>(ws);
   k_p0<<<256, 256, 0, stream>>>(ws, ip);
   k_pc<<<5120, 256, 0, stream>>>(ws, ip);
+  k_pn<<<512, 256, 0, stream>>>(ws, ip);
+  k_pn2<<<1, 64, 0, stream>>>(ws);
   k_gbig<<<32768, 256, 0, stream>>>((const float*)d_in[0], (const float*)d_in[25],
                                     (const float*)d_in[26], ws + OFF_Z, ws + OFF_FLAG);
 
   for (int t = 0; t < 128; t++) {
-    if (t) k_s0<<<1, 256, 0, stream>>>(ws);
+    if (t) k_K0<<<97, 256, 0, stream>>>(ws, t);
     k_s1<<<1280, 256, 0, stream>>>(ws, t);
     k_s2<<<776, 256, 0, stream>>>(ws, t);
-    k_s3<<<1792, 256, 0, stream>>>(ws);
+    k_s3<<<1792, 256, 0, stream>>>(ws, t);
     k_s4<<<1288, 256, 0, stream>>>(ws, t);
-    k_s5<<<1056, 256, 0, stream>>>(ws);
-    k_s6<<<696, 256, 0, stream>>>(ws);
+    k_s5<<<1056, 256, 0, stream>>>(ws, t);
+    k_s6<<<512, 256, 0, stream>>>(ws, t);
   }
 
   k_ln<<<8192, 256, 0, stream>>>(ws, (const float*)d_in[29], (const float*)d_in[30]);
```

Result: slower. 35.16 ms (+38.6%).
